# Kernel optimization log

Measured on AMD Instinct MI355X. Metric: run time of the kernel, lower is better.

Reference implementation:

```python
import jax, jax.numpy as jnp
from jax import lax
import numpy as np

NH = 8   # num_heads
WS = 7   # windowsize
SR = 2   # sr_ratio


def _conv(x, w, b, stride=1, padding=0, groups=1):
    y = lax.conv_general_dilated(x, w, (stride, stride), [(padding, padding)] * 2,
                                 dimension_numbers=('NCHW', 'OIHW', 'NCHW'),
                                 feature_group_count=groups)
    return y + b[None, :, None, None]


def _ln(x, g, b, eps=1e-5):
    m = x.mean(-1, keepdims=True)
    v = ((x - m) ** 2).mean(-1, keepdims=True)
    return (x - m) * lax.rsqrt(v + eps) * g + b


def _local_branch(q_, kv_img, dilation, stride, fc_w, sh_w, lc_w, lc_b, scale, H, W):
    # q_: [B,NH,N,hd]; kv_img: [B,C,H,W] with C = NH*hd
    B, C = kv_img.shape[0], kv_img.shape[1]
    hd = q_.shape[-1]
    pad_b = (-H) % stride
    pad_r = (-W) % stride
    kv = jnp.pad(kv_img, ((0, 0), (0, 0), (0, pad_b), (0, pad_r)), mode='reflect')
    nH, nW = (H + pad_b) // stride, (W + pad_r) // stride
    L = nH * nW
    # nn.Unfold(kernel=WS, stride, dilation): effective kernel == stride, so
    # windows tile exactly; sample each stride x stride tile at step `dilation`.
    kv = kv.reshape(B, C, nH, stride, nW, stride)[:, :, :, ::dilation, :, ::dilation]  # [B,C,nH,WS,nW,WS]
    kv = kv.transpose(0, 1, 3, 5, 2, 4).reshape(B, NH, hd, WS * WS, L)
    kv = kv.transpose(0, 1, 3, 4, 2).reshape(B, NH, WS * WS, L * hd)
    # AdaptiveAvgPool2d((None, hd)) on last dim of size L*hd -> hd buckets of L
    kv = kv.reshape(B, NH, WS * WS, hd, L).mean(-1)
    kv = (kv @ fc_w) @ sh_w                                  # [B,NH,49,2*hd]
    k_, v_ = kv[..., :hd], kv[..., hd:]
    attn = jax.nn.softmax(jnp.einsum('bhnd,bhkd->bhnk', q_, k_) * scale, axis=-1)
    v_img = v_.transpose(0, 1, 3, 2).reshape(B, C, WS, WS)
    v_ = v_ + _conv(v_img, lc_w, lc_b, padding=1, groups=C).reshape(B, NH, hd, WS * WS).transpose(0, 1, 3, 2)
    out = jnp.einsum('bhnk,bhkd->bhnd', attn, v_)            # [B,NH,N,hd]
    return out.transpose(0, 2, 1, 3).reshape(B, -1, C)


def setup_inputs() -> dict:
    key = jax.random.key(0)
    ks = jax.random.split(key, 24)
    B, H, W, dim = 2, 112, 112, 512
    N = H * W
    d0, d1, hd = 64, 224, 28
    dl = dim - d0  # 448

    def w(k, shape):
        return jax.random.normal(k, shape, jnp.float32) * 0.02

    return dict(
        x=jax.random.normal(ks[0], (B, N, dim), jnp.float32),
        Wq=w(ks[1], (dim, dim)),
        Wkv_g=w(ks[2], (d0, 2 * d0)),
        sr_w=w(ks[3], (d0, d0, SR, SR)), sr_b=w(ks[4], (d0,)),
        ln_g=jnp.ones((d0,), jnp.float32), ln_b=jnp.zeros((d0,), jnp.float32),
        lcg_w=w(ks[5], (d0, 1, 3, 3)), lcg_b=w(ks[6], (d0,)),
        kvl_dw=w(ks[7], (dl, 1, 3, 3)), kvl_db=w(ks[8], (dl,)),
        kvl_pw=w(ks[9], (dl, dl, 1, 1)), kvl_pb=w(ks[10], (dl,)),
        fc1_w=w(ks[11], (hd, hd)), sh1_w=w(ks[12], (hd, 2 * hd)),
        lc1_w=w(ks[13], (d1, 1, 3, 3)), lc1_b=w(ks[14], (d1,)),
        fc2_w=w(ks[15], (hd, hd)), sh2_w=w(ks[16], (hd, 2 * hd)),
        lc2_w=w(ks[17], (d1, 1, 3, 3)), lc2_b=w(ks[18], (d1,)),
        proj_w=w(ks[19], (dim, dim)), proj_b=w(ks[20], (dim,)),
        H=H, W=W,
    )


def reference(x, Wq, Wkv_g, sr_w, sr_b, ln_g, ln_b, lcg_w, lcg_b, kvl_dw, kvl_db,
              kvl_pw, kvl_pb, fc1_w, sh1_w, lc1_w, lc1_b, fc2_w, sh2_w, lc2_w, lc2_b,
              proj_w, proj_b, H, W):
    B, N, C = x.shape
    d0 = 64
    dl = C - d0        # 448
    hd = 224 // NH     # 28
    q = x @ Wq
    # ---- global spatially-reduced branch (1 head, dim 64) ----
    q_g = q[:, :, :d0]                                      # [B,N,64]
    x_g = x[:, :, :d0].transpose(0, 2, 1).reshape(B, d0, H, W)
    x_g = _conv(x_g, sr_w, sr_b, stride=SR)                 # [B,64,H/2,W/2]
    Hs, Ws_ = H // SR, W // SR
    Nr = Hs * Ws_
    x_g = _ln(x_g.reshape(B, d0, Nr).transpose(0, 2, 1), ln_g, ln_b)
    kvg = x_g @ Wkv_g
    k_g, v_g = kvg[..., :d0], kvg[..., d0:]
    attn_g = jax.nn.softmax(jnp.einsum('bnd,bmd->bnm', q_g, k_g) * d0 ** -0.5, axis=-1)
    v_img = v_g.transpose(0, 2, 1).reshape(B, d0, Hs, Ws_)
    v_g = v_g + _conv(v_img, lcg_w, lcg_b, padding=1, groups=d0).reshape(B, d0, Nr).transpose(0, 2, 1)
    out_g = jnp.einsum('bnm,bmd->bnd', attn_g, v_g)         # [B,N,64]
    # ---- local windowed branches (8 heads, dim 224 each) ----
    q_l = q[:, :, d0:].reshape(B, N, NH, -1).transpose(0, 2, 1, 3)  # [B,NH,N,56]
    x_l = x[:, :, d0:].reshape(B, H, W, dl).transpose(0, 3, 1, 2)
    kv_l = _conv(_conv(x_l, kvl_dw, kvl_db, padding=1, groups=dl), kvl_pw, kvl_pb)
    scale = hd ** -0.5
    out1 = _local_branch(q_l[:, :, :, :hd], kv_l[:, :224], 1, WS,
                         fc1_w, sh1_w, lc1_w, lc1_b, scale, H, W)
    out2 = _local_branch(q_l[:, :, :, hd:], kv_l[:, 224:], SR, SR * (WS - 1) + 1,
                         fc2_w, sh2_w, lc2_w, lc2_b, scale, H, W)
    return jnp.concatenate([out_g, out1, out2], -1) @ proj_w + proj_b
```

## Files before the change

kernel.cpp:

```cpp
#include <hip/hip_runtime.h>
#include <hip/hip_bf16.h>
#include <math.h>
#include <stdint.h>

static constexpr int B_    = 2;
static constexpr int N_    = 12544;
static constexpr int DIM_  = 512;
static constexpr int D0_   = 64;
static constexpr int DL_   = 448;
static constexpr int Himg  = 112;
static constexpr int Wimg  = 112;
static constexpr int HS_   = 56;
static constexpr int NR_   = 3136;
static constexpr int NH_   = 8;
static constexpr int HD_   = 28;
static constexpr int NSPLIT = 8;

typedef unsigned short ushort_t;
typedef __attribute__((ext_vector_type(8))) short short8_t;
typedef __attribute__((ext_vector_type(4))) float float4v;
typedef __attribute__((ext_vector_type(4))) unsigned uint4v;
typedef __attribute__((ext_vector_type(2))) unsigned uint2v;

static __device__ inline ushort_t bf16r(float x) {
    unsigned u = __builtin_bit_cast(unsigned, x);
    u = (u + 0x7FFFu + ((u >> 16) & 1u)) >> 16;
    return (ushort_t)u;
}
static __device__ inline float bf16tof(ushort_t h) {
    unsigned u = ((unsigned)h) << 16;
    return __builtin_bit_cast(float, u);
}
static __device__ inline unsigned pack_bf16(float lo, float hi) {
    unsigned a = __builtin_bit_cast(unsigned, lo);
    unsigned b = __builtin_bit_cast(unsigned, hi);
    a = (a + 0x7FFFu + ((a >> 16) & 1u)) >> 16;
    b = (b + 0x7FFFu + ((b >> 16) & 1u)) >> 16;
    return a | (b << 16);
}
static __device__ inline unsigned cvtpk(float lo, float hi) {
    float2 f2; f2.x = lo; f2.y = hi;
    __hip_bfloat162 h = __float22bfloat162_rn(f2);
    unsigned u;
    __builtin_memcpy(&u, &h, 4);
    return u;
}

using gptr_t = const __attribute__((address_space(1))) void*;
using lptr_t = __attribute__((address_space(3))) void*;
static __device__ inline void gload16(const void* g, void* l) {
    __builtin_amdgcn_global_load_lds((gptr_t)(uintptr_t)g, (lptr_t)(uintptr_t)l, 16, 0, 0);
}

template<bool HASBIAS, bool OUT16>
__global__ __launch_bounds__(256, 2)
void gemm_bf16_kernel(const ushort_t* __restrict__ A,
                      const ushort_t* __restrict__ Bt,
                      const float* __restrict__ bias,
                      void* __restrict__ Cv,
                      int Nn, int K, int ldc) {
    constexpr int BM = 128, BK = 64;
    __shared__ __align__(16) ushort_t As[BM * BK];
    __shared__ __align__(16) ushort_t Bs[BM * BK];
    const int bm = blockIdx.x * BM;
    const int bn = blockIdx.y * BM;
    const int tid = threadIdx.x;
    const int l15 = tid & 15;
    const int g   = (tid & 63) >> 4;
    const int w   = tid >> 6;
    const int wr  = w >> 1, wc = w & 1;

    float4v acc[4][4];
    #pragma unroll
    for (int m = 0; m < 4; ++m)
        #pragma unroll
        for (int n = 0; n < 4; ++n) acc[m][n] = (float4v){0.f, 0.f, 0.f, 0.f};

    for (int k0 = 0; k0 < K; k0 += BK) {
        #pragma unroll
        for (int i = 0; i < 4; ++i) {
            int c = i * 256 + tid;
            int r = c >> 3, ch = c & 7;
            int sch = ch ^ (r & 7);
            gload16(A  + (size_t)(bm + r) * K + k0 + sch * 8, (void*)(As + c * 8));
            gload16(Bt + (size_t)(bn + r) * K + k0 + sch * 8, (void*)(Bs + c * 8));
        }
        __syncthreads();

        short8_t af[4][2], bfr[4][2];
        #pragma unroll
        for (int m = 0; m < 4; ++m) {
            int ar = wr * 64 + m * 16 + l15;
            #pragma unroll
            for (int h = 0; h < 2; ++h)
                af[m][h] = *(const short8_t*)((const char*)As + ar * 128 + (((h * 4 + g) ^ (ar & 7)) * 16));
        }
        #pragma unroll
        for (int n = 0; n < 4; ++n) {
            int br = wc * 64 + n * 16 + l15;
            #pragma unroll
            for (int h = 0; h < 2; ++h)
                bfr[n][h] = *(const short8_t*)((const char*)Bs + br * 128 + (((h * 4 + g) ^ (br & 7)) * 16));
        }
        #pragma unroll
        for (int m = 0; m < 4; ++m)
            #pragma unroll
            for (int n = 0; n < 4; ++n) {
                acc[m][n] = __builtin_amdgcn_mfma_f32_16x16x32_bf16(af[m][0], bfr[n][0], acc[m][n], 0, 0, 0);
                acc[m][n] = __builtin_amdgcn_mfma_f32_16x16x32_bf16(af[m][1], bfr[n][1], acc[m][n], 0, 0, 0);
            }
        __syncthreads();
    }

    #pragma unroll
    for (int n = 0; n < 4; ++n) {
        int ccol = bn + wc * 64 + n * 16 + l15;
        if (ccol < Nn) {
            float bv = HASBIAS ? bias[ccol] : 0.f;
            #pragma unroll
            for (int m = 0; m < 4; ++m) {
                int crow = bm + wr * 64 + m * 16 + g * 4;
                #pragma unroll
                for (int j = 0; j < 4; ++j) {
                    float v = acc[m][n][j] + bv;
                    if (OUT16)
                        ((ushort_t*)Cv)[(size_t)(crow + j) * ldc + ccol] = bf16r(v);
                    else
                        ((float*)Cv)[(size_t)(crow + j) * ldc + ccol] = v;
                }
            }
        }
    }
}

__global__ __launch_bounds__(256)
void convw_kernel(const float* __restrict__ W, ushort_t* __restrict__ Wt,
                  int K, int Nn, int transpose) {
    int idx = blockIdx.x * 256 + threadIdx.x;
    int n = idx / K, k = idx % K;
    float v = 0.f;
    if (n < Nn) v = transpose ? W[(size_t)k * Nn + n] : W[(size_t)n * K + k];
    Wt[idx] = bf16r(v);
}

__global__ __launch_bounds__(256)
void srwt_kernel(const float* __restrict__ W, float* __restrict__ wT) {
    int idx = blockIdx.x * 256 + threadIdx.x;
    int f = idx >> 6, o = idx & 63;
    wT[idx] = W[o * 256 + f];
}

__global__ __launch_bounds__(256)
void convx_kernel(const float* __restrict__ in, ushort_t* __restrict__ outp) {
    int i = blockIdx.x * 256 + threadIdx.x;
    const float4v* p = (const float4v*)(in + (size_t)i * 8);
    float4v a = p[0], b = p[1];
    uint4v u;
    u[0] = pack_bf16(a[0], a[1]);
    u[1] = pack_bf16(a[2], a[3]);
    u[2] = pack_bf16(b[0], b[1]);
    u[3] = pack_bf16(b[2], b[3]);
    *(uint4v*)(outp + (size_t)i * 8) = u;
}

__global__ __launch_bounds__(64)
void srlnkv_kernel(const float* __restrict__ x,
                   const float* __restrict__ wT, const float* __restrict__ sr_b,
                   const float* __restrict__ ln_g, const float* __restrict__ ln_b,
                   const float* __restrict__ wkv,
                   ushort_t* __restrict__ kgb, float* __restrict__ vg) {
    const int pos = blockIdx.x;
    const int b = pos / NR_, n = pos % NR_;
    const int y = n / HS_, xx = n % HS_;
    const int o = threadIdx.x;
    __shared__ float xs[4][64];
    __shared__ float lnv_s[64];
    #pragma unroll
    for (int tap = 0; tap < 4; ++tap) {
        int ky = tap / 2, kx = tap % 2;
        xs[tap][o] = x[((size_t)b * N_ + (2 * y + ky) * Wimg + 2 * xx + kx) * DIM_ + o];
    }
    __syncthreads();
    float sum = sr_b[o];
    for (int i = 0; i < 64; ++i) {
        const float* wr = wT + (i * 4) * 64 + o;
        sum += xs[0][i] * wr[0] + xs[1][i] * wr[64] + xs[2][i] * wr[128] + xs[3][i] * wr[192];
    }
    float m = sum;
    #pragma unroll
    for (int off = 1; off < 64; off <<= 1) m += __shfl_xor(m, off);
    m *= (1.0f / 64.0f);
    float d = sum - m;
    float v = d * d;
    #pragma unroll
    for (int off = 1; off < 64; off <<= 1) v += __shfl_xor(v, off);
    v *= (1.0f / 64.0f);
    float lnv = d * rsqrtf(v + 1e-5f) * ln_g[o] + ln_b[o];
    lnv_s[o] = lnv;
    __syncthreads();
    float s0 = 0.f, s1 = 0.f;
    for (int i = 0; i < 64; ++i) {
        float lv = lnv_s[i];
        s0 += lv * wkv[i * 128 + o];
        s1 += lv * wkv[i * 128 + o + 64];
    }
    const float SCK = 0.125f * 1.44269504088896340736f;
    kgb[((size_t)b * NR_ + n) * 64 + o] = bf16r(s0 * SCK);
    vg[((size_t)b * NR_ + n) * 64 + o] = s1;
}

__global__ __launch_bounds__(256)
void lcg_kernel(const float* __restrict__ vg, const float* __restrict__ w,
                const float* __restrict__ bias, float* __restrict__ vg2) {
    int idx = blockIdx.x * 256 + threadIdx.x;
    if (idx >= B_ * NR_ * 64) return;
    int c = idx % 64;
    int n = (idx / 64) % NR_;
    int b = idx / (64 * NR_);
    int y = n / HS_, xx = n % HS_;
    float sum = vg[idx] + bias[c];
    #pragma unroll
    for (int ky = 0; ky < 3; ++ky)
        #pragma unroll
        for (int kx = 0; kx < 3; ++kx) {
            int yy = y + ky - 1, x2 = xx + kx - 1;
            if (yy >= 0 && yy < HS_ && x2 >= 0 && x2 < HS_)
                sum += vg[((size_t)b * NR_ + yy * HS_ + x2) * 64 + c] * w[c * 9 + ky * 3 + kx];
        }
    vg2[idx] = sum;
}

__global__ __launch_bounds__(256)
void vtrans_kernel(const float* __restrict__ vg2, ushort_t* __restrict__ vtb) {
    __shared__ float ld[64][65];
    const int b = blockIdx.y, n0 = blockIdx.x * 64, tid = threadIdx.x;
    #pragma unroll
    for (int i = 0; i < 16; ++i) {
        int idx = i * 256 + tid;
        int n = idx >> 6, c = idx & 63;
        ld[n][c] = vg2[((size_t)b * NR_ + n0 + n) * 64 + c];
    }
    __syncthreads();
    #pragma unroll
    for (int i = 0; i < 16; ++i) {
        int idx = i * 256 + tid;
        int d = idx >> 6, nn = idx & 63;
        vtb[(size_t)(b * 64 + d) * NR_ + n0 + nn] = bf16r(ld[nn][d]);
    }
}

__global__ __launch_bounds__(256)
void attn_global_split2(const ushort_t* __restrict__ q16,
                        const ushort_t* __restrict__ kgb,
                        const ushort_t* __restrict__ vtb,
                        ushort_t* __restrict__ osp16, float* __restrict__ mls) {
    __shared__ __align__(16) ushort_t Ks[64 * 64];
    __shared__ __align__(16) ushort_t Vs[64 * 64];
    const int split = blockIdx.y & 7;
    const int b     = blockIdx.y >> 3;
    const int q0    = blockIdx.x * 64;
    const int tid   = threadIdx.x;
    const int w     = tid >> 6;
    const int l     = tid & 63;
    const int l15   = l & 15;
    const int g     = l >> 4;
    const int lx    = l15 & 7;

    short8_t qf[2];
    {
        const ushort_t* qrow = q16 + ((size_t)b * N_ + q0 + w * 16 + l15) * DIM_;
        qf[0] = *(const short8_t*)(qrow + g * 8);
        qf[1] = *(const short8_t*)(qrow + g * 8 + 32);
    }

    float4v o[4];
    #pragma unroll
    for (int i = 0; i < 4; ++i) o[i] = (float4v){0.f, 0.f, 0.f, 0.f};
    float m_run = -3.0e38f, l_run = 0.f;

    const int t0 = (split * 49) / 8;
    const int t1 = ((split + 1) * 49) / 8;
    for (int t = t0; t < t1; ++t) {
        const int k0 = t * 64;
        #pragma unroll
        for (int i = 0; i < 2; ++i) {
            int c = i * 256 + tid;
            int r = c >> 3, ch = c & 7;
            int sch = ch ^ (r & 7);
            int pr = (r & 32) | (((r >> 2) & 3) << 3) | (((r >> 4) & 1) << 2) | (r & 3);
            gload16(kgb + ((size_t)(b * NR_ + k0 + pr) << 6) + sch * 8, (void*)(Ks + c * 8));
            gload16(vtb + (size_t)(b * 64 + r) * NR_ + k0 + sch * 8, (void*)(Vs + c * 8));
        }
        __syncthreads();

        float4v sc[4];
        #pragma unroll
        for (int c = 0; c < 4; ++c) {
            float4v acc = (float4v){0.f, 0.f, 0.f, 0.f};
            #pragma unroll
            for (int dc = 0; dc < 2; ++dc) {
                int row = c * 16 + l15;
                short8_t ak = *(const short8_t*)((const char*)Ks + row * 128 + (((g + 4 * dc) ^ lx) * 16));
                acc = __builtin_amdgcn_mfma_f32_16x16x32_bf16(ak, qf[dc], acc, 0, 0, 0);
            }
            sc[c] = acc;
        }

        float tmax = fmaxf(fmaxf(fmaxf(sc[0][0], sc[0][1]), fmaxf(sc[0][2], sc[0][3])),
                           fmaxf(fmaxf(sc[1][0], sc[1][1]), fmaxf(sc[1][2], sc[1][3])));
        tmax = fmaxf(tmax, fmaxf(fmaxf(fmaxf(sc[2][0], sc[2][1]), fmaxf(sc[2][2], sc[2][3])),
                                 fmaxf(fmaxf(sc[3][0], sc[3][1]), fmaxf(sc[3][2], sc[3][3]))));
        tmax = fmaxf(tmax, __shfl_xor(tmax, 16));
        tmax = fmaxf(tmax, __shfl_xor(tmax, 32));

        if (__any(tmax > m_run + 11.0f)) {
            float m_new = fmaxf(m_run, tmax);
            float corr = __builtin_amdgcn_exp2f(m_run - m_new);
            float co[4];
            #pragma unroll
            for (int r = 0; r < 4; ++r) co[r] = __shfl(corr, g * 4 + r);
            #pragma unroll
            for (int dc = 0; dc < 4; ++dc)
                #pragma unroll
                for (int r = 0; r < 4; ++r) o[dc][r] *= co[r];
            l_run *= corr;
            m_run = m_new;
        }

        float p[4][4];
        float ladd = 0.f;
        #pragma unroll
        for (int c = 0; c < 4; ++c)
            #pragma unroll
            for (int r = 0; r < 4; ++r) {
                float pe = __builtin_amdgcn_exp2f(sc[c][r] - m_run);
                p[c][r] = pe;
                ladd += pe;
            }
        ladd += __shfl_xor(ladd, 16);
        ladd += __shfl_xor(ladd, 32);
        l_run += ladd;

        #pragma unroll
        for (int kkc = 0; kkc < 2; ++kkc) {
            uint4v au;
            au[0] = cvtpk(p[2 * kkc][0],     p[2 * kkc][1]);
            au[1] = cvtpk(p[2 * kkc][2],     p[2 * kkc][3]);
            au[2] = cvtpk(p[2 * kkc + 1][0], p[2 * kkc + 1][1]);
            au[3] = cvtpk(p[2 * kkc + 1][2], p[2 * kkc + 1][3]);
            short8_t ap = __builtin_bit_cast(short8_t, au);
            #pragma unroll
            for (int dc = 0; dc < 4; ++dc) {
                int vrow = dc * 16 + l15;
                short8_t bv = *(const short8_t*)((const char*)Vs + vrow * 128 + (((kkc * 4 + g) ^ lx) * 16));
                o[dc] = __builtin_amdgcn_mfma_f32_16x16x32_bf16(ap, bv, o[dc], 0, 0, 0);
            }
        }
        __syncthreads();
    }

    const size_t rbase = (size_t)(split * B_ + b) * N_;
    #pragma unroll
    for (int dc = 0; dc < 4; ++dc)
        #pragma unroll
        for (int r = 0; r < 4; ++r) {
            int row = q0 + w * 16 + g * 4 + r;
            osp16[(rbase + row) * 64 + dc * 16 + l15] = bf16r(o[dc][r]);
        }
    if (l < 16) {
        int row = q0 + w * 16 + l15;
        mls[(rbase + row) * 2]     = m_run;
        mls[(rbase + row) * 2 + 1] = l_run;
    }
}

__global__ __launch_bounds__(256)
void attn_combine(const ushort_t* __restrict__ osp16, const float* __restrict__ mls,
                  ushort_t* __restrict__ catb) {
    int idx = blockIdx.x * 256 + threadIdx.x;
    int col = idx & 63;
    size_t rn = (size_t)(idx >> 6);
    const size_t BN = (size_t)B_ * N_;
    float ms[NSPLIT], ls[NSPLIT];
    float m = -3.0e38f;
    #pragma unroll
    for (int s = 0; s < NSPLIT; ++s) {
        ms[s] = mls[(s * BN + rn) * 2];
        ls[s] = mls[(s * BN + rn) * 2 + 1];
        m = fmaxf(m, ms[s]);
    }
    float lsum = 0.f, acc = 0.f;
    #pragma unroll
    for (int s = 0; s < NSPLIT; ++s) {
        float wgt = __builtin_amdgcn_exp2f(ms[s] - m);
        lsum += ls[s] * wgt;
        acc  += bf16tof(osp16[(s * BN + rn) * 64 + col]) * wgt;
    }
    catb[rn * DIM_ + col] = bf16r(acc / lsum);
}

__global__ __launch_bounds__(256)
void dwt_kernel(const float* __restrict__ x, const float* __restrict__ w,
                const float* __restrict__ bias, ushort_t* __restrict__ out) {
    int idx = blockIdx.x * 256 + threadIdx.x;
    int c4 = idx % 112;
    int t1 = idx / 112;
    int xx = t1 % 112;
    int t2 = t1 / 112;
    int yg = t2 % 28;
    int b  = t2 / 28;
    int c0 = c4 * 4;
    int y0 = yg * 4;

    float4v w4[9];
    #pragma unroll
    for (int kt = 0; kt < 9; ++kt) {
        w4[kt][0] = w[(c0 + 0) * 9 + kt];
        w4[kt][1] = w[(c0 + 1) * 9 + kt];
        w4[kt][2] = w[(c0 + 2) * 9 + kt];
        w4[kt][3] = w[(c0 + 3) * 9 + kt];
    }
    float4v bv = *(const float4v*)(bias + c0);
    float4v acc[4];
    #pragma unroll
    for (int o2 = 0; o2 < 4; ++o2) acc[o2] = bv;

    #pragma unroll
    for (int yy = 0; yy < 6; ++yy) {
        int Y = y0 - 1 + yy;
        if (Y < 0 || Y >= Himg) continue;
        #pragma unroll
        for (int xt = 0; xt < 3; ++xt) {
            int X = xx - 1 + xt;
            if (X < 0 || X >= Wimg) continue;
            float4v v = *(const float4v*)(x + ((size_t)b * N_ + Y * Wimg + X) * DIM_ + D0_ + c0);
            constexpr int olo_t[6] = {0, 0, 0, 1, 2, 3};
            constexpr int ohi_t[6] = {0, 1, 2, 3, 3, 3};
            #pragma unroll
            for (int o2 = olo_t[yy]; o2 <= ohi_t[yy]; ++o2) {
                float4v wv = w4[(yy - o2) * 3 + xt];
                acc[o2][0] += v[0] * wv[0];
                acc[o2][1] += v[1] * wv[1];
                acc[o2][2] += v[2] * wv[2];
                acc[o2][3] += v[3] * wv[3];
            }
        }
    }
    #pragma unroll
    for (int o2 = 0; o2 < 4; ++o2) {
        uint2v pk;
        pk[0] = pack_bf16(acc[o2][0], acc[o2][1]);
        pk[1] = pack_bf16(acc[o2][2], acc[o2][3]);
        *(uint2v*)(out + ((size_t)b * N_ + (y0 + o2) * Wimg + xx) * DL_ + c0) = pk;
    }
}

template<int L, int NBW, int STRIDE, int DIL, int CHOFF>
__global__ void local_mean2_kernel(const float* __restrict__ kvl,
                                   float* __restrict__ kvm) {
    __shared__ float slo[L], shi[L];
    const int blk = blockIdx.x;
    const int n = blk % 49;
    const int h = (blk / 49) % NH_;
    const int b = blk / (49 * NH_);
    const int wy = n / 7, wx = n % 7;
    const int t = threadIdx.x;

    if (t < L) {
        const int by = t / NBW, bx = t % NBW;
        int Y = by * STRIDE + DIL * wy;
        int X = bx * STRIDE + DIL * wx;
        if (Y >= Himg) Y = 2 * Himg - 2 - Y;
        if (X >= Wimg) X = 2 * Wimg - 2 - X;
        const float* src = kvl + ((size_t)b * N_ + Y * Wimg + X) * DL_ + CHOFF + h * HD_;
        float v[28];
        #pragma unroll
        for (int i = 0; i < 7; ++i) {
            float4v q4 = ((const float4v*)src)[i];
            v[i * 4] = q4[0]; v[i * 4 + 1] = q4[1]; v[i * 4 + 2] = q4[2]; v[i * 4 + 3] = q4[3];
        }
        const int f0 = t * HD_;
        const int bin0 = f0 / L;
        const int nlo = min(HD_, (bin0 + 1) * L - f0);
        float s0 = 0.f, s1 = 0.f;
        #pragma unroll
        for (int j = 0; j < HD_; ++j) {
            if (j < nlo) s0 += v[j]; else s1 += v[j];
        }
        slo[t] = s0;
        shi[t] = s1;
    }
    __syncthreads();
    if (t < HD_) {
        const int t_lo = (t * L) / HD_;
        const int t_hi = min(L - 1, (t * L + L - 1) / HD_);
        float sum = 0.f;
        for (int u = t_lo; u <= t_hi; ++u) {
            int f0 = u * HD_;
            int b0 = f0 / L;
            int b1 = (f0 + HD_ - 1) / L;
            if (b0 == t) sum += slo[u];
            if (b1 == t && b1 != b0) sum += shi[u];
        }
        kvm[(size_t)blk * HD_ + t] = sum * (1.0f / (float)L);
    }
}

__global__ __launch_bounds__(64)
void fcsh_kernel(const float* __restrict__ kvm, const float* __restrict__ fcw,
                 const float* __restrict__ shw, float* __restrict__ out) {
    int bh = blockIdx.x;
    __shared__ float kin[49][28];
    __shared__ float tmp[49][28];
    __shared__ float fw[28 * 28];
    __shared__ float sw[28 * 56];
    int t = threadIdx.x;
    for (int i = t; i < 49 * 28; i += 64) kin[i / 28][i % 28] = kvm[bh * 49 * 28 + i];
    for (int i = t; i < 28 * 28; i += 64) fw[i] = fcw[i];
    for (int i = t; i < 28 * 56; i += 64) sw[i] = shw[i];
    __syncthreads();
    for (int i = t; i < 49 * 28; i += 64) {
        int rr = i / 28, j = i % 28;
        float s = 0.f;
        for (int k = 0; k < 28; ++k) s += kin[rr][k] * fw[k * 28 + j];
        tmp[rr][j] = s;
    }
    __syncthreads();
    for (int i = t; i < 49 * 56; i += 64) {
        int rr = i / 56, j = i % 56;
        float s = 0.f;
        for (int k = 0; k < 28; ++k) s += tmp[rr][k] * sw[k * 56 + j];
        out[bh * 49 * 56 + i] = s;
    }
}

__global__ __launch_bounds__(256)
void vconv_kernel(const float* __restrict__ kvsh, const float* __restrict__ w,
                  const float* __restrict__ bias, float* __restrict__ vc) {
    int idx = blockIdx.x * 256 + threadIdx.x;
    if (idx >= B_ * NH_ * 49 * HD_) return;
    int d  = idx % HD_;
    int n  = (idx / HD_) % 49;
    int bh = idx / (HD_ * 49);
    int h  = bh % NH_;
    int y = n / 7, xx = n % 7;
    int c = h * HD_ + d;
    float sum = kvsh[(bh * 49 + n) * 56 + 28 + d] + bias[c];
    #pragma unroll
    for (int ky = 0; ky < 3; ++ky)
        #pragma unroll
        for (int kx = 0; kx < 3; ++kx) {
            int yy = y + ky - 1, x2 = xx + kx - 1;
            if (yy >= 0 && yy < 7 && x2 >= 0 && x2 < 7)
                sum += kvsh[(bh * 49 + yy * 7 + x2) * 56 + 28 + d] * w[c * 9 + ky * 3 + kx];
        }
    vc[idx] = sum;
}

__global__ __launch_bounds__(256)
void attn_local_mfma(const ushort_t* __restrict__ q16,
                     const float* __restrict__ kv1, const float* __restrict__ v1c,
                     const float* __restrict__ kv2, const float* __restrict__ v2c,
                     ushort_t* __restrict__ catb) {
    __shared__ __align__(16) ushort_t Ks[64 * 32];
    __shared__ __align__(16) ushort_t Vt[32 * 64];
    const int ybh    = blockIdx.y;
    const int branch = ybh & 1;
    const int bh     = ybh >> 1;
    const int b      = bh >> 3, h = bh & 7;
    const int q0     = blockIdx.x * 64;
    const int tid    = threadIdx.x;
    const int w      = tid >> 6;
    const int l      = tid & 63;
    const int l15    = l & 15;
    const int g      = l >> 4;
    const float SC2K = 0.1889822365046136f * 1.44269504088896340736f;

    const float* kvsh = branch ? kv2 : kv1;
    const float* vc   = branch ? v2c : v1c;
    const int qoff    = D0_ + h * 56 + branch * 28;
    const int outoff  = (branch ? D0_ + 224 : D0_) + h * HD_;

    {
        int row = tid >> 2, lc = tid & 3;
        int pr = (row & 32) | (((row >> 2) & 3) << 3) | (((row >> 4) & 1) << 2) | (row & 3);
        uint4v u = (uint4v){0u, 0u, 0u, 0u};
        if (pr < 49) {
            const float* src = kvsh + (bh * 49 + pr) * 56 + lc * 8;
            float vv[8];
            #pragma unroll
            for (int j2 = 0; j2 < 8; ++j2)
                vv[j2] = (lc * 8 + j2 < 28) ? src[j2] * SC2K : 0.f;
            u[0] = cvtpk(vv[0], vv[1]);
            u[1] = cvtpk(vv[2], vv[3]);
            u[2] = cvtpk(vv[4], vv[5]);
            u[3] = cvtpk(vv[6], vv[7]);
        }
        *(uint4v*)(Ks + row * 32 + (lc ^ (row & 3)) * 8) = u;
    }
    {
        int row = tid >> 3, lc = tid & 7;
        uint4v u = (uint4v){0u, 0u, 0u, 0u};
        if (row < 28) {
            float vv[8];
            #pragma unroll
            for (int j2 = 0; j2 < 8; ++j2) {
                int kc = lc * 8 + j2;
                vv[j2] = (kc < 49) ? vc[(bh * 49 + kc) * 28 + row] : 0.f;
            }
            u[0] = cvtpk(vv[0], vv[1]);
            u[1] = cvtpk(vv[2], vv[3]);
            u[2] = cvtpk(vv[4], vv[5]);
            u[3] = cvtpk(vv[6], vv[7]);
        }
        *(uint4v*)(Vt + row * 64 + (lc ^ (row & 7)) * 8) = u;
    }
    short8_t qf;
    {
        const ushort_t* qp = q16 + ((size_t)b * N_ + q0 + w * 16 + l15) * DIM_ + qoff + g * 8;
        uint2v a01 = *(const uint2v*)qp;
        uint2v a23 = (g < 3) ? *(const uint2v*)(qp + 4) : (uint2v){0u, 0u};
        uint4v uv;
        uv[0] = a01[0]; uv[1] = a01[1]; uv[2] = a23[0]; uv[3] = a23[1];
        qf = __builtin_bit_cast(short8_t, uv);
    }
    __syncthreads();

    float4v sc4[4];
    #pragma unroll
    for (int c = 0; c < 4; ++c) {
        int row = c * 16 + l15;
        short8_t ak = *(const short8_t*)(Ks + row * 32 + ((g ^ (row & 3)) * 8));
        float4v acc = (float4v){0.f, 0.f, 0.f, 0.f};
        sc4[c] = __builtin_amdgcn_mfma_f32_16x16x32_bf16(ak, qf, acc, 0, 0, 0);
    }

    float tmax = fmaxf(fmaxf(fmaxf(sc4[0][0], sc4[0][1]), fmaxf(sc4[0][2], sc4[0][3])),
                       fmaxf(fmaxf(sc4[1][0], sc4[1][1]), fmaxf(sc4[1][2], sc4[1][3])));
    tmax = fmaxf(tmax, fmaxf(fmaxf(fmaxf(sc4[2][0], sc4[2][1]), fmaxf(sc4[2][2], sc4[2][3])),
                             fmaxf(fmaxf(sc4[3][0], sc4[3][1]), fmaxf(sc4[3][2], sc4[3][3]))));
    tmax = fmaxf(tmax, __shfl_xor(tmax, 16));
    tmax = fmaxf(tmax, __shfl_xor(tmax, 32));

    float p[4][4];
    float lsum = 0.f;
    #pragma unroll
    for (int c = 0; c < 4; ++c)
        #pragma unroll
        for (int r = 0; r < 4; ++r) {
            float pe = __builtin_amdgcn_exp2f(sc4[c][r] - tmax);
            if (c >= 2 && (8 * g + 4 * (c & 1) + r) >= 17) pe = 0.f;
            p[c][r] = pe;
            lsum += pe;
        }
    lsum += __shfl_xor(lsum, 16);
    lsum += __shfl_xor(lsum, 32);
    float inv = 1.0f / lsum;

    float4v o2[2];
    o2[0] = (float4v){0.f, 0.f, 0.f, 0.f};
    o2[1] = (float4v){0.f, 0.f, 0.f, 0.f};
    #pragma unroll
    for (int kkc = 0; kkc < 2; ++kkc) {
        uint4v au;
        au[0] = cvtpk(p[2 * kkc][0],     p[2 * kkc][1]);
        au[1] = cvtpk(p[2 * kkc][2],     p[2 * kkc][3]);
        au[2] = cvtpk(p[2 * kkc + 1][0], p[2 * kkc + 1][1]);
        au[3] = cvtpk(p[2 * kkc + 1][2], p[2 * kkc + 1][3]);
        short8_t ap = __builtin_bit_cast(short8_t, au);
        #pragma unroll
        for (int dc = 0; dc < 2; ++dc) {
            int vrow = dc * 16 + l15;
            short8_t bv = *(const short8_t*)(Vt + vrow * 64 + (((kkc * 4 + g) ^ (vrow & 7)) * 8));
            o2[dc] = __builtin_amdgcn_mfma_f32_16x16x32_bf16(ap, bv, o2[dc], 0, 0, 0);
        }
    }

    float irow[4];
    #pragma unroll
    for (int r = 0; r < 4; ++r) irow[r] = __shfl(inv, g * 4 + r);
    #pragma unroll
    for (int dc = 0; dc < 2; ++dc) {
        int d = dc * 16 + l15;
        if (d < 28) {
            #pragma unroll
            for (int r = 0; r < 4; ++r) {
                int row = q0 + w * 16 + g * 4 + r;
                catb[((size_t)b * N_ + row) * DIM_ + outoff + d] = bf16r(o2[dc][r] * irow[r]);
            }
        }
    }
}

extern "C" void kernel_launch(void* const* d_in, const int* in_sizes, int n_in,
                              void* d_out, int out_size, void* d_ws, size_t ws_size,
                              hipStream_t stream) {
    const float* x      = (const float*)d_in[0];
    const float* Wq     = (const float*)d_in[1];
    const float* Wkv_g  = (const float*)d_in[2];
    const float* sr_w   = (const float*)d_in[3];
    const float* sr_b   = (const float*)d_in[4];
    const float* ln_g   = (const float*)d_in[5];
    const float* ln_b   = (const float*)d_in[6];
    const float* lcg_w  = (const float*)d_in[7];
    const float* lcg_b  = (const float*)d_in[8];
    const float* kvl_dw = (const float*)d_in[9];
    const float* kvl_db = (const float*)d_in[10];
    const float* kvl_pw = (const float*)d_in[11];
    const float* kvl_pb = (const float*)d_in[12];
    const float* fc1_w  = (const float*)d_in[13];
    const float* sh1_w  = (const float*)d_in[14];
    const float* lc1_w  = (const float*)d_in[15];
    const float* lc1_b  = (const float*)d_in[16];
    const float* fc2_w  = (const float*)d_in[17];
    const float* sh2_w  = (const float*)d_in[18];
    const float* lc2_w  = (const float*)d_in[19];
    const float* lc2_b  = (const float*)d_in[20];
    const float* proj_w = (const float*)d_in[21];
    const float* proj_b = (const float*)d_in[22];
    float* out = (float*)d_out;
    char* base = (char*)d_ws;

    size_t o = 0;
    auto alloc = [&](size_t bytes) -> void* {
        void* p = base + o;
        o = (o + bytes + 255) & ~(size_t)255;
        return p;
    };
    ushort_t* q16   = (ushort_t*)alloc((size_t)B_ * N_ * DIM_ * 2);
    float*    kvl   = (float*)   alloc((size_t)B_ * N_ * DL_ * 4);
    ushort_t* xcat  = (ushort_t*)alloc((size_t)B_ * N_ * DIM_ * 2);
    ushort_t* dwtb  = (ushort_t*)alloc((size_t)B_ * N_ * DL_ * 2);
    ushort_t* kgb   = (ushort_t*)alloc((size_t)B_ * NR_ * 64 * 2);
    float*    vg    = (float*)   alloc((size_t)B_ * NR_ * 64 * 4);
    float*    vg2   = (float*)   alloc((size_t)B_ * NR_ * 64 * 4);
    ushort_t* vtb   = (ushort_t*)alloc((size_t)B_ * 64 * NR_ * 2);
    ushort_t* wqt   = (ushort_t*)alloc((size_t)512 * 512 * 2);
    ushort_t* pwt   = (ushort_t*)alloc((size_t)512 * 448 * 2);
    ushort_t* projt = (ushort_t*)alloc((size_t)512 * 512 * 2);
    float*    srwt  = (float*)   alloc((size_t)256 * 64 * 4);
    float*    kvm1  = (float*)   alloc((size_t)B_ * NH_ * 49 * HD_ * 4);
    float*    kvm2  = (float*)   alloc((size_t)B_ * NH_ * 49 * HD_ * 4);
    float*    kv1   = (float*)   alloc((size_t)B_ * NH_ * 49 * 56 * 4);
    float*    kv2   = (float*)   alloc((size_t)B_ * NH_ * 49 * 56 * 4);
    float*    v1c   = (float*)   alloc((size_t)B_ * NH_ * 49 * HD_ * 4);
    float*    v2c   = (float*)   alloc((size_t)B_ * NH_ * 49 * HD_ * 4);
    ushort_t* xbf  = xcat;
    ushort_t* catb = xcat;
    ushort_t* osp16 = (ushort_t*)kvl;
    float*    mls   = (float*)((char*)kvl + (size_t)NSPLIT * B_ * N_ * 64 * 2);

    const int M = B_ * N_;

    convw_kernel<<<512 * 512 / 256, 256, 0, stream>>>(Wq, wqt, 512, 512, 1);
    convw_kernel<<<512 * 448 / 256, 256, 0, stream>>>(kvl_pw, pwt, 448, 448, 0);
    convw_kernel<<<512 * 512 / 256, 256, 0, stream>>>(proj_w, projt, 512, 512, 1);
    srwt_kernel<<<64, 256, 0, stream>>>(sr_w, srwt);
    convx_kernel<<<(B_ * N_ * DIM_ / 8) / 256, 256, 0, stream>>>(x, xbf);

    gemm_bf16_kernel<false, true><<<dim3(M / 128, 4), 256, 0, stream>>>(
        xbf, wqt, nullptr, q16, 512, 512, 512);

    dwt_kernel<<<(B_ * 28 * 112 * 112) / 256, 256, 0, stream>>>(x, kvl_dw, kvl_db, dwtb);

    gemm_bf16_kernel<true, false><<<dim3(M / 128, 4), 256, 0, stream>>>(
        dwtb, pwt, kvl_pb, kvl, 448, 448, 448);

    srlnkv_kernel<<<B_ * NR_, 64, 0, stream>>>(x, srwt, sr_b, ln_g, ln_b, Wkv_g, kgb, vg);

    lcg_kernel<<<(B_ * NR_ * 64) / 256, 256, 0, stream>>>(vg, lcg_w, lcg_b, vg2);
    vtrans_kernel<<<dim3(NR_ / 64, B_), 256, 0, stream>>>(vg2, vtb);

    {
        local_mean2_kernel<256, 16, 7, 1, 0><<<B_ * NH_ * 49, 256, 0, stream>>>(kvl, kvm1);
        local_mean2_kernel<81, 9, 13, 2, 224><<<B_ * NH_ * 49, 128, 0, stream>>>(kvl, kvm2);
        fcsh_kernel<<<B_ * NH_, 64, 0, stream>>>(kvm1, fc1_w, sh1_w, kv1);
        fcsh_kernel<<<B_ * NH_, 64, 0, stream>>>(kvm2, fc2_w, sh2_w, kv2);
        int tot = B_ * NH_ * 49 * HD_;
        int blocks = (tot + 255) / 256;
        vconv_kernel<<<blocks, 256, 0, stream>>>(kv1, lc1_w, lc1_b, v1c);
        vconv_kernel<<<blocks, 256, 0, stream>>>(kv2, lc2_w, lc2_b, v2c);
    }

    attn_global_split2<<<dim3(N_ / 64, B_ * NSPLIT), 256, 0, stream>>>(q16, kgb, vtb, osp16, mls);
    attn_combine<<<(B_ * N_ * 64) / 256, 256, 0, stream>>>(osp16, mls, catb);

    attn_local_mfma<<<dim3(N_ / 64, B_ * NH_ * 2), 256, 0, stream>>>(
        q16, kv1, v1c, kv2, v2c, catb);

    gemm_bf16_kernel<true, false><<<dim3(M / 128, 4), 256, 0, stream>>>(
        catb, projt, proj_b, out, 512, 512, 512);
}
```

Before: 311.8 us.

## Stage two K/V tiles per barrier and defer row-sum shuffles in global attention

The global attention split kernel now loads two 64-key K/V tiles into doubled LDS buffers before a single barrier, then processes both, which halves the number of barrier pairs per split. The cross-lane shuffles that reduce the row max now run only inside the rare rescale branch, and the row-sum shuffle reduction moves out of the loop to a single pass at the end. This trades extra LDS (32KB per block), which may reduce occupancy, for fewer barriers and fewer shuffles. The loads are still not overlapped with compute.

```diff
diff --git a/kernel.cpp b/kernel.cpp
--- a/kernel.cpp
+++ b/kernel.cpp
@@ -254,8 +254,8 @@
                         const ushort_t* __restrict__ kgb,
                         const ushort_t* __restrict__ vtb,
                         ushort_t* __restrict__ osp16, float* __restrict__ mls) {
-    __shared__ __align__(16) ushort_t Ks[64 * 64];
-    __shared__ __align__(16) ushort_t Vs[64 * 64];
+    __shared__ __align__(16) ushort_t Ks[2 * 64 * 64];
+    __shared__ __align__(16) ushort_t Vs[2 * 64 * 64];
     const int split = blockIdx.y & 7;
     const int b     = blockIdx.y >> 3;
     const int q0    = blockIdx.x * 64;
@@ -278,21 +278,30 @@
     for (int i = 0; i < 4; ++i) o[i] = (float4v){0.f, 0.f, 0.f, 0.f};
     float m_run = -3.0e38f, l_run = 0.f;
 
-    const int t0 = (split * 49) / 8;
-    const int t1 = ((split + 1) * 49) / 8;
-    for (int t = t0; t < t1; ++t) {
+    int stg_c[2], stg_r[2], stg_sch[2], stg_pr[2];
+    #pragma unroll
+    for (int i = 0; i < 2; ++i) {
+        int c = i * 256 + tid;
+        int r = c >> 3, ch = c & 7;
+        stg_c[i] = c;
+        stg_r[i] = r;
+        stg_sch[i] = ch ^ (r & 7);
+        stg_pr[i] = (r & 32) | (((r >> 2) & 3) << 3) | (((r >> 4) & 1) << 2) | (r & 3);
+    }
+    auto stage = [&](int t, int buf) {
         const int k0 = t * 64;
+        ushort_t* kd = Ks + buf * 4096;
+        ushort_t* vd = Vs + buf * 4096;
         #pragma unroll
         for (int i = 0; i < 2; ++i) {
-            int c = i * 256 + tid;
-            int r = c >> 3, ch = c & 7;
-            int sch = ch ^ (r & 7);
-            int pr = (r & 32) | (((r >> 2) & 3) << 3) | (((r >> 4) & 1) << 2) | (r & 3);
-            gload16(kgb + ((size_t)(b * NR_ + k0 + pr) << 6) + sch * 8, (void*)(Ks + c * 8));
-            gload16(vtb + (size_t)(b * 64 + r) * NR_ + k0 + sch * 8, (void*)(Vs + c * 8));
-        }
-        __syncthreads();
-
+            gload16(kgb + ((size_t)(b * NR_ + k0 + stg_pr[i]) << 6) + stg_sch[i] * 8,
+                    (void*)(kd + stg_c[i] * 8));
+            gload16(vtb + (size_t)(b * 64 + stg_r[i]) * NR_ + k0 + stg_sch[i] * 8,
+                    (void*)(vd + stg_c[i] * 8));
+        }
+    };
+
+    auto compute = [&](const ushort_t* Kb, const ushort_t* Vb) {
         float4v sc[4];
         #pragma unroll
         for (int c = 0; c < 4; ++c) {
@@ -300,7 +309,7 @@
             #pragma unroll
             for (int dc = 0; dc < 2; ++dc) {
                 int row = c * 16 + l15;
-                short8_t ak = *(const short8_t*)((const char*)Ks + row * 128 + (((g + 4 * dc) ^ lx) * 16));
+                short8_t ak = *(const short8_t*)((const char*)Kb + row * 128 + (((g + 4 * dc) ^ lx) * 16));
                 acc = __builtin_amdgcn_mfma_f32_16x16x32_bf16(ak, qf[dc], acc, 0, 0, 0);
             }
             sc[c] = acc;
@@ -310,11 +319,11 @@
                            fmaxf(fmaxf(sc[1][0], sc[1][1]), fmaxf(sc[1][2], sc[1][3])));
         tmax = fmaxf(tmax, fmaxf(fmaxf(fmaxf(sc[2][0], sc[2][1]), fmaxf(sc[2][2], sc[2][3])),
                                  fmaxf(fmaxf(sc[3][0], sc[3][1]), fmaxf(sc[3][2], sc[3][3]))));
-        tmax = fmaxf(tmax, __shfl_xor(tmax, 16));
-        tmax = fmaxf(tmax, __shfl_xor(tmax, 32));
 
         if (__any(tmax > m_run + 11.0f)) {
-            float m_new = fmaxf(m_run, tmax);
+            float rmax = fmaxf(tmax, __shfl_xor(tmax, 16));
+            rmax = fmaxf(rmax, __shfl_xor(rmax, 32));
+            float m_new = fmaxf(m_run, rmax);
             float corr = __builtin_amdgcn_exp2f(m_run - m_new);
             float co[4];
             #pragma unroll
@@ -337,8 +346,6 @@
                 p[c][r] = pe;
                 ladd += pe;
             }
-        ladd += __shfl_xor(ladd, 16);
-        ladd += __shfl_xor(ladd, 32);
         l_run += ladd;
 
         #pragma unroll
@@ -352,12 +359,32 @@
             #pragma unroll
             for (int dc = 0; dc < 4; ++dc) {
                 int vrow = dc * 16 + l15;
-                short8_t bv = *(const short8_t*)((const char*)Vs + vrow * 128 + (((kkc * 4 + g) ^ lx) * 16));
+                short8_t bv = *(const short8_t*)((const char*)Vb + vrow * 128 + (((kkc * 4 + g) ^ lx) * 16));
                 o[dc] = __builtin_amdgcn_mfma_f32_16x16x32_bf16(ap, bv, o[dc], 0, 0, 0);
             }
         }
+    };
+
+    const int t0 = (split * 49) / 8;
+    const int t1 = ((split + 1) * 49) / 8;
+    int t = t0;
+    for (; t + 1 < t1; t += 2) {
+        stage(t, 0);
+        stage(t + 1, 1);
         __syncthreads();
-    }
+        compute(Ks, Vs);
+        compute(Ks + 4096, Vs + 4096);
+        __syncthreads();
+    }
+    if (t < t1) {
+        stage(t, 0);
+        __syncthreads();
+        compute(Ks, Vs);
+    }
+
+    float l_tot = l_run;
+    l_tot += __shfl_xor(l_tot, 16);
+    l_tot += __shfl_xor(l_tot, 32);
 
     const size_t rbase = (size_t)(split * B_ + b) * N_;
     #pragma unroll
@@ -370,7 +397,7 @@
     if (l < 16) {
         int row = q0 + w * 16 + l15;
         mls[(rbase + row) * 2]     = m_run;
-        mls[(rbase + row) * 2 + 1] = l_run;
+        mls[(rbase + row) * 2 + 1] = l_tot;
     }
 }
 
```

Result: no change. 306.4 us (-1.7%).
